# Kernel tuning notes

Measured on AMD Instinct MI355X. Metric: run time of the kernel, lower is better.

## Reference

```python
import jax, jax.numpy as jnp
import numpy as np

CD_W1 = 1.0
CD_W2 = 1.0


def setup_inputs() -> dict:
    key = jax.random.key(0)
    k1, k2 = jax.random.split(key)
    B, N, M, D = 16, 4096, 4096, 3
    points1 = jax.random.normal(k1, (B, N, D), dtype=jnp.float32)
    points2 = jax.random.normal(k2, (B, M, D), dtype=jnp.float32)
    return {"points1": points1, "points2": points2}


def reference(points1, points2):
    # squared pairwise distances via |a|^2 + |b|^2 - 2 a.b (GEMM form)
    a2 = jnp.sum(points1 * points1, axis=-1)          # [B, N]
    b2 = jnp.sum(points2 * points2, axis=-1)          # [B, M]
    ab = jnp.einsum("bnd,bmd->bnm", points1, points2)  # [B, N, M]
    dist = a2[:, :, None] + b2[:, None, :] - 2.0 * ab   # [B, N, M]
    dist_min1 = jnp.min(dist, axis=2)                  # nearest in points2 for each point1
    dist_min2 = jnp.min(dist, axis=1)                  # nearest in points1 for each point2
    B = points1.shape[0]
    return (CD_W1 * jnp.sum(dist_min1) + CD_W2 * jnp.sum(dist_min2)) / B
```

## Files before the change

### kernel.cpp

```cpp
#include <hip/hip_runtime.h>

#define BQ     16
#define NPTS   4096
#define TOTAL  (BQ * NPTS)
#define NPART  128

#define ROWMIN_FLOATS ((size_t)8 * TOTAL)
#define WS_NEED (ROWMIN_FLOATS * 4 + (size_t)NPART * 4)

typedef __attribute__((ext_vector_type(8)))  short short8;
typedef __attribute__((ext_vector_type(16))) float f32x16;

__device__ __forceinline__ unsigned short f2bf(float x) {
    union { float f; unsigned u; } v; v.f = x;
    unsigned r = v.u + 0x7FFFu + ((v.u >> 16) & 1u);
    return (unsigned short)(r >> 16);
}
__device__ __forceinline__ float bf2f(unsigned short h) {
    union { float f; unsigned u; } v; v.u = ((unsigned)h) << 16; return v.f;
}
#define BF_ONE 0x3F80

__device__ __forceinline__ uint4 make_bslots(const float* __restrict__ pts,
                                             int tile, int lane) {
    const int pidx = lane & 31, g = lane >> 5;
    const float* pp = pts + (size_t)(tile * 32 + pidx) * 3;
    const float x = pp[0], y = pp[1], z = pp[2];
    const unsigned short xh = f2bf(x), yh = f2bf(y), zh = f2bf(z);
    const unsigned short xl = f2bf(x - bf2f(xh)), yl = f2bf(y - bf2f(yh)),
                         zl = f2bf(z - bf2f(zh));
    const unsigned short m2xh = f2bf(-2.0f * bf2f(xh)), m2yh = f2bf(-2.0f * bf2f(yh)),
                         m2zh = f2bf(-2.0f * bf2f(zh));
    const unsigned short m2xl = f2bf(-2.0f * bf2f(xl)), m2yl = f2bf(-2.0f * bf2f(yl)),
                         m2zl = f2bf(-2.0f * bf2f(zl));
    const float s2 = fmaf(x, x, fmaf(y, y, z * z));
    const unsigned short s2h = f2bf(s2);
    const unsigned short s2l = f2bf(s2 - bf2f(s2h));
    unsigned short s[8];
    if (g == 0) { s[0]=m2xh; s[1]=m2yh; s[2]=m2zh; s[3]=m2xl; s[4]=m2yl; s[5]=m2zl; s[6]=m2xh; s[7]=m2yh; }
    else        { s[0]=m2zh; s[1]=BF_ONE; s[2]=BF_ONE; s[3]=s2h; s[4]=s2l; s[5]=0; s[6]=0; s[7]=0; }
    uint4 o;
    o.x = (unsigned)s[0] | ((unsigned)s[1] << 16);
    o.y = (unsigned)s[2] | ((unsigned)s[3] << 16);
    o.z = (unsigned)s[4] | ((unsigned)s[5] << 16);
    o.w = (unsigned)s[6] | ((unsigned)s[7] << 16);
    return o;
}

__device__ __forceinline__ short8 make_aslots(const float* __restrict__ pts,
                                              int point, int g) {
    const float* pp = pts + (size_t)point * 3;
    const float x = pp[0], y = pp[1], z = pp[2];
    const unsigned short xh = f2bf(x), yh = f2bf(y), zh = f2bf(z);
    const unsigned short xl = f2bf(x - bf2f(xh)), yl = f2bf(y - bf2f(yh)),
                         zl = f2bf(z - bf2f(zh));
    const float s2 = fmaf(x, x, fmaf(y, y, z * z));
    const unsigned short s2h = f2bf(s2);
    const unsigned short s2l = f2bf(s2 - bf2f(s2h));
    unsigned short s[8];
    if (g == 0) { s[0]=xh; s[1]=yh; s[2]=zh; s[3]=xh; s[4]=yh; s[5]=zh; s[6]=xl; s[7]=yl; }
    else        { s[0]=zl; s[1]=s2h; s[2]=s2l; s[3]=BF_ONE; s[4]=BF_ONE; s[5]=0; s[6]=0; s[7]=0; }
    union { unsigned u[4]; short8 v; } o;
    o.u[0] = (unsigned)s[0] | ((unsigned)s[1] << 16);
    o.u[1] = (unsigned)s[2] | ((unsigned)s[3] << 16);
    o.u[2] = (unsigned)s[4] | ((unsigned)s[5] << 16);
    o.u[3] = (unsigned)s[6] | ((unsigned)s[7] << 16);
    return o.v;
}

__global__ __launch_bounds__(256, 4) void cd_main(
        const float* __restrict__ p1, const float* __restrict__ p2,
        float* __restrict__ rowmin) {
    const int dir  = blockIdx.y;
    const float* __restrict__ A  = dir ? p2 : p1;
    const float* __restrict__ Bp = dir ? p1 : p2;

    const int bx   = blockIdx.x;
    const int b    = bx >> 6;
    const int rg   = (bx >> 2) & 15;
    const int cg   = bx & 3;
    const int wave = threadIdx.x >> 6;
    const int lane = threadIdx.x & 63;
    const int pidx = lane & 31, g = lane >> 5;

    __shared__ uint4 spanel[32 * 64];

    const float* __restrict__ Bbase = Bp + (size_t)(b * NPTS + cg * 1024) * 3;
#pragma unroll
    for (int k = 0; k < 8; ++k) {
        const int s = threadIdx.x + k * 256;
        spanel[s] = make_bslots(Bbase, s >> 6, s & 63);
    }

    const int rowbase = b * NPTS + rg * 256 + wave * 64;

    const short8 a0 = make_aslots(A, rowbase      + pidx, g);
    const short8 a1 = make_aslots(A, rowbase + 32 + pidx, g);

    f32x16 zero, r0, r1;
#pragma unroll
    for (int e = 0; e < 16; ++e) { zero[e] = 0.0f; r0[e] = 3.0e38f; r1[e] = 3.0e38f; }

    __syncthreads();

#define CD_COMPUTE(C0, C1)                                                    \
    do {                                                                      \
        const short8 bf0 = *reinterpret_cast<const short8*>(&(C0));           \
        const short8 bf1 = *reinterpret_cast<const short8*>(&(C1));           \
        f32x16 d0, d1;                                                        \
        d0 = __builtin_amdgcn_mfma_f32_32x32x16_bf16(a0, bf0, zero, 0, 0, 0); \
        d1 = __builtin_amdgcn_mfma_f32_32x32x16_bf16(a0, bf1, zero, 0, 0, 0); \
        _Pragma("unroll") for (int e = 0; e < 16; ++e)                        \
            r0[e] = fminf(r0[e], fminf(d0[e], d1[e]));                        \
        d0 = __builtin_amdgcn_mfma_f32_32x32x16_bf16(a1, bf0, zero, 0, 0, 0); \
        d1 = __builtin_amdgcn_mfma_f32_32x32x16_bf16(a1, bf1, zero, 0, 0, 0); \
        _Pragma("unroll") for (int e = 0; e < 16; ++e)                        \
            r1[e] = fminf(r1[e], fminf(d0[e], d1[e]));                        \
    } while (0)

    int t0 = wave * 8;
    uint4 c0 = spanel[t0 * 64 + lane], c1 = spanel[(t0 + 1) * 64 + lane];
#pragma unroll 1
    for (int i = 0; i < 15; ++i) {
        const int tn = (t0 + 2) & 31;
        uint4 n0 = spanel[tn * 64 + lane];
        uint4 n1 = spanel[(tn + 1) * 64 + lane];
        CD_COMPUTE(c0, c1);
        c0 = n0; c1 = n1; t0 = tn;
    }
    CD_COMPUTE(c0, c1);
#undef CD_COMPUTE

    float* __restrict__ outr = rowmin + (size_t)(dir * 4 + cg) * TOTAL;
#pragma unroll
    for (int e = 0; e < 16; ++e) {
        float v0 = r0[e], v1 = r1[e];
#pragma unroll
        for (int m = 1; m <= 16; m <<= 1) {
            v0 = fminf(v0, __shfl_xor(v0, m));
            v1 = fminf(v1, __shfl_xor(v1, m));
        }
        const int rl = (e & 3) + 8 * (e >> 2) + 4 * g;
        if (pidx == 0) {
            outr[rowbase +      rl] = fmaxf(v0, 0.0f);
            outr[rowbase + 32 + rl] = fmaxf(v1, 0.0f);
        }
    }
}

__global__ __launch_bounds__(256) void cd_combine(const float* __restrict__ rowmin,
                                                  float* __restrict__ partial) {
    __shared__ float sred[256];
    const int tid = blockIdx.x * 256 + threadIdx.x;
    float s = 0.0f;
#pragma unroll
    for (int k = 0; k < 4; ++k) {
        const int i   = tid + k * 32768;
        const int d   = i >> 16;
        const int row = i & (TOTAL - 1);
        const float* base = rowmin + (size_t)d * 4 * TOTAL + row;
        s += fminf(fminf(base[0], base[TOTAL]),
                   fminf(base[2 * TOTAL], base[3 * TOTAL]));
    }
    sred[threadIdx.x] = s;
    __syncthreads();
    for (int st = 128; st > 0; st >>= 1) {
        if (threadIdx.x < st) sred[threadIdx.x] += sred[threadIdx.x + st];
        __syncthreads();
    }
    if (threadIdx.x == 0) partial[blockIdx.x] = sred[0];
}

__global__ __launch_bounds__(NPART) void cd_final(const float* __restrict__ partial,
                                                  float* __restrict__ out) {
    __shared__ float sred[NPART];
    sred[threadIdx.x] = partial[threadIdx.x];
    __syncthreads();
    for (int st = NPART / 2; st > 0; st >>= 1) {
        if (threadIdx.x < st) sred[threadIdx.x] += sred[threadIdx.x + st];
        __syncthreads();
    }
    if (threadIdx.x == 0) out[0] = sred[0] * (1.0f / (float)BQ);
}

__global__ __launch_bounds__(256) void cd_init_ws(unsigned int* __restrict__ ws) {
    ws[blockIdx.x * 256 + threadIdx.x] = 0x7F800000u;
}
#define F_APT 8
__global__ __launch_bounds__(256) void cd_min_lds(
        const float* __restrict__ p1, const float* __restrict__ p2,
        unsigned int* __restrict__ wsmin) {
    const int dir = blockIdx.y;
    const float* __restrict__ Aset = dir ? p2 : p1;
    const float* __restrict__ Bset = dir ? p1 : p2;
    unsigned int* __restrict__ outmin = wsmin + dir * TOTAL;
    const int atile = blockIdx.x / 16;
    const int mtile = blockIdx.x % 16;
    const int a0 = atile * 2048;
    const int m0 = (a0 / NPTS) * NPTS + mtile * 256;
    __shared__ float4 sbf[256];
    {
        const float* bpn = Bset + (size_t)(m0 + threadIdx.x) * 3;
        float bx = bpn[0], by = bpn[1], bz = bpn[2];
        sbf[threadIdx.x] = make_float4(-2.0f*bx, -2.0f*by, -2.0f*bz,
                                       fmaf(bx,bx,fmaf(by,by,bz*bz)));
    }
    __syncthreads();
    float ax[F_APT], ay[F_APT], az_[F_APT], q2[F_APT], mn[F_APT];
#pragma unroll
    for (int k = 0; k < F_APT; ++k) {
        const int ai = a0 + k*256 + threadIdx.x;
        const float* ap = Aset + (size_t)ai * 3;
        ax[k]=ap[0]; ay[k]=ap[1]; az_[k]=ap[2];
        q2[k]=fmaf(ax[k],ax[k],fmaf(ay[k],ay[k],az_[k]*az_[k]));
        mn[k]=3.0e38f;
    }
#pragma unroll 2
    for (int j = 0; j < 256; j += 2) {
        const float4 b0 = sbf[j], b1 = sbf[j+1];
#pragma unroll
        for (int k = 0; k < F_APT; ++k) {
            float d0 = fmaf(az_[k],b0.z,b0.w); d0=fmaf(ay[k],b0.y,d0); d0=fmaf(ax[k],b0.x,d0);
            float d1 = fmaf(az_[k],b1.z,b1.w); d1=fmaf(ay[k],b1.y,d1); d1=fmaf(ax[k],b1.x,d1);
            mn[k] = fminf(fminf(mn[k], d0), d1);
        }
    }
#pragma unroll
    for (int k = 0; k < F_APT; ++k) {
        const int ai = a0 + k*256 + threadIdx.x;
        atomicMin(&outmin[ai], __float_as_uint(fmaxf(q2[k]+mn[k], 0.0f)));
    }
}
__global__ __launch_bounds__(1024) void cd_reduce_single(const float* __restrict__ wsmin,
                                                         float* __restrict__ out) {
    __shared__ float sred[1024];
    const float4* __restrict__ v = (const float4*)wsmin;
    float s = 0.0f;
    for (int i = threadIdx.x; i < (2*TOTAL)/4; i += 1024) {
        float4 x = v[i]; s += (x.x + x.y) + (x.z + x.w);
    }
    sred[threadIdx.x] = s;
    __syncthreads();
    for (int st = 512; st > 0; st >>= 1) {
        if (threadIdx.x < st) sred[threadIdx.x] += sred[threadIdx.x + st];
        __syncthreads();
    }
    if (threadIdx.x == 0) out[0] = sred[0] * (1.0f / (float)BQ);
}

extern "C" void kernel_launch(void* const* d_in, const int* in_sizes, int n_in,
                              void* d_out, int out_size, void* d_ws, size_t ws_size,
                              hipStream_t stream) {
    const float* p1 = (const float*)d_in[0];
    const float* p2 = (const float*)d_in[1];
    float* out = (float*)d_out;

    if (ws_size >= WS_NEED) {
        float* rowmin  = (float*)d_ws;
        float* partial = (float*)((char*)d_ws + ROWMIN_FLOATS * 4);

        dim3 grid(1024, 2, 1);
        cd_main<<<grid, 256, 0, stream>>>(p1, p2, rowmin);
        cd_combine<<<128, 256, 0, stream>>>(rowmin, partial);
        cd_final<<<1, NPART, 0, stream>>>(partial, out);
    } else {
        unsigned* wsmin = (unsigned*)d_ws;
        cd_init_ws<<<(2 * TOTAL) / 256, 256, 0, stream>>>(wsmin);
        dim3 grid(512, 2, 1);
        cd_min_lds<<<grid, 256, 0, stream>>>(p1, p2, wsmin);
        cd_reduce_single<<<1, 1024, 0, stream>>>((const float*)wsmin, out);
    }
}
```

Baseline: 40.58 us.

## Precompute bf16 MFMA operand fragments in a separate prep kernel

Adds a cd_prep kernel that converts both point sets once into packed bf16 hi/lo operand fragments (B panels and A fragments) stored in workspace. cd_main then loads these prebuilt uint4 slots instead of re-deriving them from float coordinates in every block, removing redundant conversion work (each B panel was rebuilt by 16 row-group blocks). The launch-bounds occupancy hint also drops from 4 to 3 blocks per CU. This costs an extra kernel launch plus extra workspace traffic and a larger workspace requirement, which could push execution into the fallback path if the workspace is too small.

```diff
diff --git a/kernel.cpp b/kernel.cpp
--- a/kernel.cpp
+++ b/kernel.cpp
@@ -5,8 +5,12 @@
 #define TOTAL  (BQ * NPTS)
 #define NPART  128
 
+#define PANEL_U4_SIDE ((size_t)131072)
+#define AFRAG_U4_SIDE ((size_t)131072)
+#define PANELS_BYTES  ((size_t)2 * PANEL_U4_SIDE * 16)
+#define AFRAGS_BYTES  ((size_t)2 * AFRAG_U4_SIDE * 16)
 #define ROWMIN_FLOATS ((size_t)8 * TOTAL)
-#define WS_NEED (ROWMIN_FLOATS * 4 + (size_t)NPART * 4)
+#define WS_NEED (PANELS_BYTES + AFRAGS_BYTES + ROWMIN_FLOATS * 4 + (size_t)NPART * 4)
 
 typedef __attribute__((ext_vector_type(8)))  short short8;
 typedef __attribute__((ext_vector_type(16))) float f32x16;
@@ -47,8 +51,8 @@
     return o;
 }
 
-__device__ __forceinline__ short8 make_aslots(const float* __restrict__ pts,
-                                              int point, int g) {
+__device__ __forceinline__ uint4 make_aslots_u4(const float* __restrict__ pts,
+                                                int point, int g) {
     const float* pp = pts + (size_t)point * 3;
     const float x = pp[0], y = pp[1], z = pp[2];
     const unsigned short xh = f2bf(x), yh = f2bf(y), zh = f2bf(z);
@@ -60,20 +64,32 @@
     unsigned short s[8];
     if (g == 0) { s[0]=xh; s[1]=yh; s[2]=zh; s[3]=xh; s[4]=yh; s[5]=zh; s[6]=xl; s[7]=yl; }
     else        { s[0]=zl; s[1]=s2h; s[2]=s2l; s[3]=BF_ONE; s[4]=BF_ONE; s[5]=0; s[6]=0; s[7]=0; }
-    union { unsigned u[4]; short8 v; } o;
-    o.u[0] = (unsigned)s[0] | ((unsigned)s[1] << 16);
-    o.u[1] = (unsigned)s[2] | ((unsigned)s[3] << 16);
-    o.u[2] = (unsigned)s[4] | ((unsigned)s[5] << 16);
-    o.u[3] = (unsigned)s[6] | ((unsigned)s[7] << 16);
-    return o.v;
-}
-
-__global__ __launch_bounds__(256, 4) void cd_main(
-        const float* __restrict__ p1, const float* __restrict__ p2,
+    uint4 o;
+    o.x = (unsigned)s[0] | ((unsigned)s[1] << 16);
+    o.y = (unsigned)s[2] | ((unsigned)s[3] << 16);
+    o.z = (unsigned)s[4] | ((unsigned)s[5] << 16);
+    o.w = (unsigned)s[6] | ((unsigned)s[7] << 16);
+    return o;
+}
+
+__global__ __launch_bounds__(256) void cd_prep(const float* __restrict__ p1,
+                                               const float* __restrict__ p2,
+                                               uint4* __restrict__ panels,
+                                               uint4* __restrict__ afrags) {
+    const int tid  = blockIdx.x * 256 + threadIdx.x;
+    const int side = tid >> 17;
+    const int l    = tid & 131071;
+    const float* pts = side ? p2 : p1;
+    panels[tid] = make_bslots(pts, l >> 6, l & 63);
+    afrags[tid] = make_aslots_u4(pts, l >> 1, l & 1);
+}
+
+__global__ __launch_bounds__(256, 3) void cd_main(
+        const uint4* __restrict__ panels, const uint4* __restrict__ afrags,
         float* __restrict__ rowmin) {
     const int dir  = blockIdx.y;
-    const float* __restrict__ A  = dir ? p2 : p1;
-    const float* __restrict__ Bp = dir ? p1 : p2;
+    const uint4* __restrict__ panelB = panels + (dir ? 0 : PANEL_U4_SIDE);
+    const uint4* __restrict__ afragA = afrags + (dir ? AFRAG_U4_SIDE : 0);
 
     const int bx   = blockIdx.x;
     const int b    = bx >> 6;
@@ -85,17 +101,19 @@
 
     __shared__ uint4 spanel[32 * 64];
 
-    const float* __restrict__ Bbase = Bp + (size_t)(b * NPTS + cg * 1024) * 3;
+    const uint4* __restrict__ psrc = panelB + (size_t)(b * 128 + cg * 32) * 64;
 #pragma unroll
     for (int k = 0; k < 8; ++k) {
         const int s = threadIdx.x + k * 256;
-        spanel[s] = make_bslots(Bbase, s >> 6, s & 63);
+        spanel[s] = psrc[s];
     }
 
     const int rowbase = b * NPTS + rg * 256 + wave * 64;
 
-    const short8 a0 = make_aslots(A, rowbase      + pidx, g);
-    const short8 a1 = make_aslots(A, rowbase + 32 + pidx, g);
+    uint4 a0u = afragA[(size_t)(rowbase + pidx) * 2 + g];
+    uint4 a1u = afragA[(size_t)(rowbase + 32 + pidx) * 2 + g];
+    const short8 a0 = *reinterpret_cast<const short8*>(&a0u);
+    const short8 a1 = *reinterpret_cast<const short8*>(&a1u);
 
     f32x16 zero, r0, r1;
 #pragma unroll
@@ -256,11 +274,15 @@
     float* out = (float*)d_out;
 
     if (ws_size >= WS_NEED) {
-        float* rowmin  = (float*)d_ws;
-        float* partial = (float*)((char*)d_ws + ROWMIN_FLOATS * 4);
-
+        uint4* panels  = (uint4*)d_ws;
+        uint4* afrags  = (uint4*)((char*)d_ws + PANELS_BYTES);
+        float* rowmin  = (float*)((char*)d_ws + PANELS_BYTES + AFRAGS_BYTES);
+        float* partial = (float*)((char*)d_ws + PANELS_BYTES + AFRAGS_BYTES
+                                  + ROWMIN_FLOATS * 4);
+
+        cd_prep<<<1024, 256, 0, stream>>>(p1, p2, panels, afrags);
         dim3 grid(1024, 2, 1);
-        cd_main<<<grid, 256, 0, stream>>>(p1, p2, rowmin);
+        cd_main<<<grid, 256, 0, stream>>>(panels, afrags, rowmin);
         cd_combine<<<128, 256, 0, stream>>>(rowmin, partial);
         cd_final<<<1, NPART, 0, stream>>>(partial, out);
     } else {
```

Measured after the change: 43.37 us. +6.9%, slower.
